# Optimization experiments

Measured on AMD Instinct MI355X. Metric: run time of the kernel, lower is better.

## Reference

```python
import jax, jax.numpy as jnp
import numpy as np

NUM_EMBEDDINGS = 1024
EMBEDDING_DIM = 256
COMMITMENT_COST = 0.25
DECAY = 0.99
EPSILON = 1e-05


def setup_inputs() -> dict:
    key = jax.random.key(0)
    k1, k2, k3 = jax.random.split(key, 3)
    z = jax.random.normal(k1, (32, EMBEDDING_DIM, 32, 32), dtype=jnp.float32)
    codebook = jax.random.normal(k2, (NUM_EMBEDDINGS, EMBEDDING_DIM), dtype=jnp.float32)
    ema_cluster_size = jnp.zeros((NUM_EMBEDDINGS,), dtype=jnp.float32)
    ema_dw = jax.random.normal(k3, (NUM_EMBEDDINGS, EMBEDDING_DIM), dtype=jnp.float32)
    return {"z": z, "codebook": codebook, "ema_cluster_size": ema_cluster_size, "ema_dw": ema_dw}


def reference(z, codebook, ema_cluster_size, ema_dw):
    K, D = codebook.shape
    # (B,C,H,W) -> (B,H,W,C)
    zp = jnp.transpose(z, (0, 2, 3, 1))
    z_flat = zp.reshape(-1, D)  # [N, D]
    N = z_flat.shape[0]

    # squared L2 distances to each code: [N, K]
    distances = (jnp.sum(z_flat ** 2, axis=1, keepdims=True)
                 + jnp.sum(codebook ** 2, axis=1)
                 - 2.0 * z_flat @ codebook.T)
    idx = jnp.argmin(distances, axis=1)  # [N]

    quantized = codebook[idx].reshape(zp.shape)  # [B,H,W,C]

    # training-mode EMA codebook update (one-hot scatter expressed as segment sums)
    counts = jax.ops.segment_sum(jnp.ones((N,), z_flat.dtype), idx, num_segments=K)  # encodings.sum(0)
    dw = jax.ops.segment_sum(z_flat, idx, num_segments=K)                            # encodings.T @ z_flat
    new_cluster_size = ema_cluster_size * DECAY + (1.0 - DECAY) * counts
    new_ema_dw = ema_dw * DECAY + (1.0 - DECAY) * dw
    n = jnp.sum(new_cluster_size)
    cluster_size = (new_cluster_size + EPSILON) / (n + K * EPSILON) * n
    new_codebook = new_ema_dw / cluster_size[:, None]

    commitment_loss = jnp.mean((zp - jax.lax.stop_gradient(quantized)) ** 2)
    loss = COMMITMENT_COST * commitment_loss

    # straight-through estimator
    quantized_st = zp + jax.lax.stop_gradient(quantized - zp)

    avg_probs = counts / N
    perplexity = jnp.exp(-jnp.sum(avg_probs * jnp.log(avg_probs + 1e-10)))

    quantized_out = jnp.transpose(quantized_st, (0, 3, 1, 2))  # back to (B,C,H,W)
    return (quantized_out, loss, perplexity, new_codebook, new_cluster_size, new_ema_dw)
```

## Files before the change

### kernel.cpp

```cpp
#include <hip/hip_runtime.h>
#include <cfloat>
#include <cstdint>

#define B_BATCH 32
#define D_DIM   256
#define HW      1024
#define N_POS   32768
#define K_CODES 1024
#define DECAY_F   0.99f
#define ONE_M_DECAY 0.01f
#define EPS_F   1e-5f

#define OUT_Q    0
#define OUT_LOSS 8388608
#define OUT_PERP 8388609
#define OUT_CB   8388610
#define OUT_NCS  8650754
#define OUT_EDW  8651778


#define WS_COUNTS  0
#define WS_ZNORM   4096
#define WS_BSUM    4100
#define WS_MEMSET  4104
#define WS_CBNORM  4352
#define WS_OFFS    8448
#define WS_CURSOR  12544
#define WS_IDX     16640
#define WS_SORTED  147712
#define WS_CBHI    278784
#define WS_CBLO    803072
#define WS_PART    1327360
#define WS_SCODE   3424512
#define WS_TOTAL   3555584

typedef short s16x8 __attribute__((ext_vector_type(8)));
typedef float f32x4 __attribute__((ext_vector_type(4)));
typedef unsigned long long u64;

__device__ __forceinline__ ushort f2bf_rne(float x) {
    uint u = __float_as_uint(x);
    uint r = (u + 0x7FFF + ((u >> 16) & 1)) >> 16;
    return (ushort)r;
}
__device__ __forceinline__ float bf2f(ushort h) {
    return __uint_as_float(((uint)h) << 16);
}

__device__ __forceinline__ void gload16(const void* g, void* l) {
    __builtin_amdgcn_global_load_lds(
        (const __attribute__((address_space(1))) unsigned*)(uintptr_t)g,
        (__attribute__((address_space(3))) unsigned*)(uintptr_t)l, 16, 0, 0);
}

__global__ __launch_bounds__(256) void prep_ztrans(const float* __restrict__ z,
                                                   const float* __restrict__ cb,
                                                   ushort* __restrict__ zhi,
                                                   ushort* __restrict__ zlo,
                                                   ushort* __restrict__ cbhi,
                                                   ushort* __restrict__ cblo,
                                                   float* __restrict__ cbnorm,
                                                   float* __restrict__ znorm_acc) {
    __shared__ float Zs[32][65];
    __shared__ float red[256];
    const int tid = threadIdx.x;

    if (blockIdx.x >= 512) {
        int wave = tid >> 6;
        int lane = tid & 63;
        int k = (blockIdx.x - 512) * 4 + wave;
        float4 v = *(const float4*)&cb[(size_t)k * D_DIM + lane * 4];
        ushort4 h, l;
        h.x = f2bf_rne(v.x); l.x = f2bf_rne(v.x - bf2f(h.x));
        h.y = f2bf_rne(v.y); l.y = f2bf_rne(v.y - bf2f(h.y));
        h.z = f2bf_rne(v.z); l.z = f2bf_rne(v.z - bf2f(h.z));
        h.w = f2bf_rne(v.w); l.w = f2bf_rne(v.w - bf2f(h.w));
        *(ushort4*)&cbhi[(size_t)k * D_DIM + lane * 4] = h;
        *(ushort4*)&cblo[(size_t)k * D_DIM + lane * 4] = l;
        float s = v.x * v.x + v.y * v.y + v.z * v.z + v.w * v.w;
        #pragma unroll
        for (int off = 32; off >= 1; off >>= 1) s += __shfl_xor(s, off);
        if (lane == 0) cbnorm[k] = s;
        return;
    }

    const int n0  = blockIdx.x * 64;
    const int b   = n0 >> 10;
    const int hw0 = n0 & 1023;
    const float* zb = z + (size_t)b * (D_DIM * HW) + hw0;

    const int zn = tid & 63;
    const int zdb = (tid >> 6) * 8;
    const int n  = tid >> 2;
    const int dq = tid & 3;
    float zsum = 0.f;

    for (int d0 = 0; d0 < D_DIM; d0 += 32) {
        __syncthreads();
        #pragma unroll
        for (int j = 0; j < 8; ++j)
            Zs[zdb + j][zn] = zb[(size_t)(d0 + zdb + j) * HW + zn];
        __syncthreads();
        s16x8 hv, lv;
        #pragma unroll
        for (int j = 0; j < 8; ++j) {
            float f = Zs[dq * 8 + j][n];
            zsum += f * f;
            ushort hb = f2bf_rne(f);
            ushort lb = f2bf_rne(f - bf2f(hb));
            hv[j] = (short)hb;
            lv[j] = (short)lb;
        }
        *(s16x8*)&zhi[(size_t)(n0 + n) * D_DIM + d0 + dq * 8] = hv;
        *(s16x8*)&zlo[(size_t)(n0 + n) * D_DIM + d0 + dq * 8] = lv;
    }
    red[tid] = zsum;
    __syncthreads();
    for (int s2 = 128; s2 >= 1; s2 >>= 1) {
        if (tid < s2) red[tid] += red[tid + s2];
        __syncthreads();
    }
    if (tid == 0) atomicAdd(znorm_acc, red[0]);
}

__global__ __launch_bounds__(256) void argmin_gemm(const ushort* __restrict__ cbhi,
                                                   const ushort* __restrict__ cblo,
                                                   const ushort* __restrict__ zhi,
                                                   const ushort* __restrict__ zlo,
                                                   const float* __restrict__ cbnorm,
                                                   u64* __restrict__ partial) {
    __shared__ ushort lds[16384];
    __shared__ u64 kred[128][2];

    const int tid  = threadIdx.x;
    const int wave = tid >> 6;
    const int lane = tid & 63;
    const int col  = lane & 15;
    const int lg   = lane >> 4;
    const int blk = blockIdx.x;
    const int mt = (blk >> 3) & 7;
    const int pt = (blk & 7) | ((blk >> 6) << 3);
    const int ch = wave & 1;
    const int ph = wave >> 1;

    const int r0  = tid >> 2;
    const int dch = (tid & 3) ^ ((r0 >> 1) & 3);
    const size_t eA0 = (size_t)(mt * 128 + r0) * D_DIM + dch * 8;
    const size_t eB0 = (size_t)(pt * 128 + r0) * D_DIM + dch * 8;
    const int ldsw = wave * 512;

    const int swz = (lg ^ ((col >> 1) & 3)) * 8;
    const int soffA = (ch * 64 + col) * 32 + swz;
    const int soffB = (ph * 64 + col) * 32 + swz;

    f32x4 acc[4][4];
    #pragma unroll
    for (int mi = 0; mi < 4; ++mi)
        #pragma unroll
        for (int ni = 0; ni < 4; ++ni) acc[mi][ni] = {0.f, 0.f, 0.f, 0.f};

    for (int s8 = 0; s8 < 8; ++s8) {
        const int d0 = s8 * 32;
        __syncthreads();
        gload16(cbhi + eA0 + d0,            &lds[0     + ldsw]);
        gload16(cbhi + eA0 + 64 * 256 + d0, &lds[2048  + ldsw]);
        gload16(cblo + eA0 + d0,            &lds[4096  + ldsw]);
        gload16(cblo + eA0 + 64 * 256 + d0, &lds[6144  + ldsw]);
        gload16(zhi  + eB0 + d0,            &lds[8192  + ldsw]);
        gload16(zhi  + eB0 + 64 * 256 + d0, &lds[10240 + ldsw]);
        gload16(zlo  + eB0 + d0,            &lds[12288 + ldsw]);
        gload16(zlo  + eB0 + 64 * 256 + d0, &lds[14336 + ldsw]);
        __syncthreads();

        s16x8 ah[4], al[4], bh[4], bl[4];
        #pragma unroll
        for (int mi = 0; mi < 4; ++mi) {
            int so = soffA + mi * 512;
            ah[mi] = *(const s16x8*)&lds[so];
            al[mi] = *(const s16x8*)&lds[4096 + so];
        }
        #pragma unroll
        for (int ni = 0; ni < 4; ++ni) {
            int so = soffB + ni * 512;
            bh[ni] = *(const s16x8*)&lds[8192 + so];
            bl[ni] = *(const s16x8*)&lds[12288 + so];
        }
        #pragma unroll
        for (int mi = 0; mi < 4; ++mi)
            #pragma unroll
            for (int ni = 0; ni < 4; ++ni) {
                acc[mi][ni] = __builtin_amdgcn_mfma_f32_16x16x32_bf16(ah[mi], bh[ni], acc[mi][ni], 0, 0, 0);
                acc[mi][ni] = __builtin_amdgcn_mfma_f32_16x16x32_bf16(ah[mi], bl[ni], acc[mi][ni], 0, 0, 0);
                acc[mi][ni] = __builtin_amdgcn_mfma_f32_16x16x32_bf16(al[mi], bh[ni], acc[mi][ni], 0, 0, 0);
            }
    }

    const int kbase = mt * 128 + ch * 64;
    u64 best[4] = {~0ull, ~0ull, ~0ull, ~0ull};
    #pragma unroll
    for (int mi = 0; mi < 4; ++mi) {
        float4 cn = *(const float4*)&cbnorm[kbase + mi * 16 + lg * 4];
        const float* cnp = (const float*)&cn;
        #pragma unroll
        for (int ni = 0; ni < 4; ++ni) {
            #pragma unroll
            for (int r = 0; r < 4; ++r) {
                float dist = cnp[r] - 2.f * acc[mi][ni][r];
                uint ub = __float_as_uint(dist);
                ub = ub ^ (uint)(((int)ub >> 31) | 0x80000000);
                u64 key = ((u64)ub << 32) | (uint)(kbase + mi * 16 + lg * 4 + r);
                if (key < best[ni]) best[ni] = key;
            }
        }
    }
    #pragma unroll
    for (int ni = 0; ni < 4; ++ni) {
        u64 o = __shfl_xor(best[ni], 16); if (o < best[ni]) best[ni] = o;
        o = __shfl_xor(best[ni], 32); if (o < best[ni]) best[ni] = o;
    }
    if (lane < 16) {
        #pragma unroll
        for (int ni = 0; ni < 4; ++ni)
            kred[ph * 64 + ni * 16 + lane][ch] = best[ni];
    }
    __syncthreads();
    if (tid < 128) {
        u64 a = kred[tid][0], b = kred[tid][1];
        partial[(size_t)(pt * 128 + tid) * 8 + mt] = a < b ? a : b;
    }
}

__global__ __launch_bounds__(256) void combine_kernel(const u64* __restrict__ partial,
                                                      int* __restrict__ idx,
                                                      float* __restrict__ counts,
                                                      float* __restrict__ bsum_acc) {
    __shared__ int hist[1024];
    __shared__ float red[256];
    const int tid = threadIdx.x;
    for (int j = tid; j < 1024; j += 256) hist[j] = 0;
    __syncthreads();
    int n = blockIdx.x * 256 + tid;
    const u64* p = partial + (size_t)n * 8;
    u64 m = p[0];
    #pragma unroll
    for (int j = 1; j < 8; ++j) { u64 v = p[j]; if (v < m) m = v; }
    int k = (int)(m & 1023u);
    idx[n] = k;
    atomicAdd(&hist[k], 1);
    uint ub = (uint)(m >> 32);
    uint u = (ub & 0x80000000u) ? (ub ^ 0x80000000u) : ~ub;
    red[tid] = __uint_as_float(u);
    __syncthreads();
    for (int s2 = 128; s2 >= 1; s2 >>= 1) {
        if (tid < s2) red[tid] += red[tid + s2];
        __syncthreads();
    }
    if (tid == 0) atomicAdd(bsum_acc, red[0]);
    for (int j = tid; j < 1024; j += 256) {
        int c = hist[j];
        if (c) atomicAdd(&counts[j], (float)c);
    }
}

__global__ __launch_bounds__(1024) void small_kernel(const float* __restrict__ ema_cs,
                                                     const float* __restrict__ counts,
                                                     const float* __restrict__ znorm,
                                                     const float* __restrict__ bsum,
                                                     float* __restrict__ out_ncs,
                                                     float* __restrict__ out_perp,
                                                     float* __restrict__ out_loss,
                                                     float* __restrict__ ntot_ws,
                                                     int* __restrict__ offsets,
                                                     int* __restrict__ cursor) {
    __shared__ float s1[1024];
    __shared__ float s2[1024];
    __shared__ int   s3[1024];
    int k = threadIdx.x;
    float cnt = counts[k];
    float ncs = ema_cs[k] * DECAY_F + ONE_M_DECAY * cnt;
    out_ncs[k] = ncs;
    float p = cnt / (float)N_POS;
    s1[k] = ncs;
    s2[k] = p * logf(p + 1e-10f);
    int c = (int)cnt;
    s3[k] = c;
    __syncthreads();
    for (int off = 1; off < 1024; off <<= 1) {
        int v = (k >= off) ? s3[k - off] : 0;
        __syncthreads();
        s3[k] += v;
        __syncthreads();
    }
    int excl = s3[k] - c;
    offsets[k] = excl;
    cursor[k] = excl;
    for (int st = 512; st >= 1; st >>= 1) {
        if (k < st) { s1[k] += s1[k + st]; s2[k] += s2[k + st]; }
        __syncthreads();
    }
    if (k == 0) {
        ntot_ws[0] = s1[0];
        out_perp[0] = expf(-s2[0]);
        out_loss[0] = 0.25f * (znorm[0] + bsum[0]) / 8388608.0f;
    }
}

__global__ __launch_bounds__(256) void scatter_kernel(const int* __restrict__ idx,
                                                      int* __restrict__ cursor,
                                                      int* __restrict__ sorted,
                                                      int* __restrict__ scode,
                                                      float* __restrict__ dw_zero) {
    __shared__ int hist[1024];
    __shared__ int base_s[1024];
    const int tid = threadIdx.x;
    {
        float4 z4 = {0.f, 0.f, 0.f, 0.f};
        size_t e = ((size_t)blockIdx.x * 256 + tid) * 8;
        *(float4*)&dw_zero[e] = z4;
        *(float4*)&dw_zero[e + 4] = z4;
    }
    for (int j = tid; j < 1024; j += 256) hist[j] = 0;
    __syncthreads();
    int n = blockIdx.x * 256 + tid;
    int k = idx[n];
    atomicAdd(&hist[k], 1);
    __syncthreads();
    for (int j = tid; j < 1024; j += 256) {
        int c = hist[j];
        if (c) base_s[j] = atomicAdd(&cursor[j], c);
        hist[j] = 0;
    }
    __syncthreads();
    int rank = atomicAdd(&hist[k], 1);
    int pos = base_s[k] + rank;
    sorted[pos] = n;
    scode[pos] = k;
}

#define DW_CHUNK 64
__global__ __launch_bounds__(256) void dw_chunk_kernel(const ushort* __restrict__ zhi,
                                                       const ushort* __restrict__ zlo,
                                                       const int* __restrict__ sorted,
                                                       const int* __restrict__ scode,
                                                       const int* __restrict__ offsets,
                                                       const float* __restrict__ counts,
                                                       float* __restrict__ dw) {
    __shared__ int sid[DW_CHUNK];
    __shared__ int sk[DW_CHUNK];
    const int tid = threadIdx.x;
    const int p0 = blockIdx.x * DW_CHUNK;
    if (tid < DW_CHUNK) {
        sid[tid] = sorted[p0 + tid];
        sk[tid]  = scode[p0 + tid];
    }
    __syncthreads();
    float acc = 0.f;
    int runstart = 0;
    #pragma unroll 4
    for (int i = 0; i < DW_CHUNK; ++i) {
        int id = sid[i];
        float zv = bf2f(zhi[(size_t)id * D_DIM + tid]) + bf2f(zlo[(size_t)id * D_DIM + tid]);
        acc += zv;
        bool end = (i == DW_CHUNK - 1) || (sk[i + 1] != sk[i]);
        if (end) {
            int k = sk[i];
            int off = offsets[k];
            int cnt = (int)counts[k];
            if (p0 + runstart == off && p0 + i == off + cnt - 1)
                dw[(size_t)k * D_DIM + tid] = acc;
            else
                atomicAdd(&dw[(size_t)k * D_DIM + tid], acc);
            acc = 0.f;
            runstart = i + 1;
        }
    }
}

__global__ __launch_bounds__(256) void fuse_lite(const float* __restrict__ cb,
                                                 const int* __restrict__ idx,
                                                 float* __restrict__ outq) {
    __shared__ float Qs[32][65];
    __shared__ int kidx[64];
    const int tid = threadIdx.x;
    const int n0  = blockIdx.x * 64;
    const int b   = n0 >> 10;
    const int hw0 = n0 & 1023;
    float* ob = outq + (size_t)b * (D_DIM * HW) + hw0;

    if (tid < 64) kidx[tid] = idx[n0 + tid];

    for (int d0 = 0; d0 < D_DIM; d0 += 32) {
        __syncthreads();
        #pragma unroll
        for (int h = 0; h < 2; ++h) {
            int s  = tid + 256 * h;
            int n  = s >> 3;
            int dq = s & 7;
            int k  = kidx[n];
            float4 q = *(const float4*)&cb[(size_t)k * D_DIM + d0 + dq * 4];
            Qs[dq * 4 + 0][n] = q.x;
            Qs[dq * 4 + 1][n] = q.y;
            Qs[dq * 4 + 2][n] = q.z;
            Qs[dq * 4 + 3][n] = q.w;
        }
        __syncthreads();
        #pragma unroll
        for (int j = 0; j < 8; ++j) {
            int v = tid + 256 * j;
            int d = v >> 6;
            int n = v & 63;
            ob[(size_t)(d0 + d) * HW + n] = Qs[d][n];
        }
    }
}

__global__ __launch_bounds__(256) void finalize_rows(const float* __restrict__ ema_dw,
                                                     const float* __restrict__ out_ncs,
                                                     const float* __restrict__ ntot_ws,
                                                     float* __restrict__ out_edw,
                                                     float* __restrict__ out_cb) {
    int k = blockIdx.x;
    int d = threadIdx.x;
    float ncs = out_ncs[k];
    float nt = ntot_ws[0];
    float csz = (ncs + EPS_F) / (nt + (float)K_CODES * EPS_F) * nt;
    size_t e = (size_t)k * D_DIM + d;
    float ed = ema_dw[e] * DECAY_F + ONE_M_DECAY * out_edw[e];
    out_edw[e] = ed;
    out_cb[e] = ed / csz;
}

extern "C" void kernel_launch(void* const* d_in, const int* in_sizes, int n_in,
                              void* d_out, int out_size, void* d_ws, size_t ws_size,
                              hipStream_t stream) {
    const float* z       = (const float*)d_in[0];
    const float* cb      = (const float*)d_in[1];
    const float* ema_cs  = (const float*)d_in[2];
    const float* ema_dw  = (const float*)d_in[3];
    float* out = (float*)d_out;

    char* ws = (char*)d_ws;
    float* ws_counts = (float*)(ws + WS_COUNTS);
    float* ws_znorm  = (float*)(ws + WS_ZNORM);
    float* ws_bsum   = (float*)(ws + WS_BSUM);
    float* ws_cbnorm = (float*)(ws + WS_CBNORM);
    int*   ws_offs   = (int*)(ws + WS_OFFS);
    int*   ws_cursor = (int*)(ws + WS_CURSOR);
    int*   ws_idx    = (int*)(ws + WS_IDX);
    int*   ws_sorted = (int*)(ws + WS_SORTED);
    ushort* ws_cbhi  = (ushort*)(ws + WS_CBHI);
    ushort* ws_cblo  = (ushort*)(ws + WS_CBLO);
    u64*   ws_part   = (u64*)(ws + WS_PART);
    int*   ws_scode  = (int*)(ws + WS_SCODE);

    ushort* zhi = (ushort*)out;
    ushort* zlo = zhi + 8388608;

    hipMemsetAsync(d_ws, 0, WS_MEMSET, stream);

    prep_ztrans<<<768, 256, 0, stream>>>(z, cb, zhi, zlo, ws_cbhi, ws_cblo,
                                         ws_cbnorm, ws_znorm);
    argmin_gemm<<<2048, 256, 0, stream>>>(ws_cbhi, ws_cblo, zhi, zlo, ws_cbnorm, ws_part);
    combine_kernel<<<N_POS / 256, 256, 0, stream>>>(ws_part, ws_idx, ws_counts, ws_bsum);
    small_kernel<<<1, 1024, 0, stream>>>(ema_cs, ws_counts, ws_znorm, ws_bsum,
                                         out + OUT_NCS, out + OUT_PERP, out + OUT_LOSS,
                                         (float*)(ws + WS_ZNORM) + 1024, ws_offs, ws_cursor);
    scatter_kernel<<<N_POS / 256, 256, 0, stream>>>(ws_idx, ws_cursor, ws_sorted,
                                                    ws_scode, out + OUT_EDW);
    dw_chunk_kernel<<<N_POS / DW_CHUNK, 256, 0, stream>>>(zhi, zlo, ws_sorted, ws_scode,
                                                          ws_offs, ws_counts, out + OUT_EDW);
    fuse_lite<<<N_POS / 64, 256, 0, stream>>>(cb, ws_idx, out + OUT_Q);
    finalize_rows<<<K_CODES, 256, 0, stream>>>(ema_dw, out + OUT_NCS,
                                               (float*)(ws + WS_ZNORM) + 1024,
                                               out + OUT_EDW, out + OUT_CB);
}
```

Baseline: 216.1 us.

## Triple-buffer argmin GEMM with larger 256x128 tiles and 512-thread blocks

Restructures the split-bf16 distance GEMM to use 512-thread blocks covering 256 codes by 128 positions, with K-steps of 32 bf16 elements. Global-to-LDS loads go through a three-stage ring buffer using explicit vmcnt waits and raw barriers, so loads for later steps overlap with MFMA work. MFMA sections also run at raised wave priority. Each position now has half as many partial argmin candidates, so the combine kernel reads 4 instead of 8. The cost is about 144KB of LDS per block, which limits occupancy, and more fragile hand-written wait counts.

```diff
diff --git a/kernel.cpp b/kernel.cpp
--- a/kernel.cpp
+++ b/kernel.cpp
@@ -123,35 +123,49 @@
     if (tid == 0) atomicAdd(znorm_acc, red[0]);
 }
 
-__global__ __launch_bounds__(256) void argmin_gemm(const ushort* __restrict__ cbhi,
-                                                   const ushort* __restrict__ cblo,
-                                                   const ushort* __restrict__ zhi,
-                                                   const ushort* __restrict__ zlo,
-                                                   const float* __restrict__ cbnorm,
-                                                   u64* __restrict__ partial) {
-    __shared__ ushort lds[16384];
-    __shared__ u64 kred[128][2];
+__global__ __launch_bounds__(512, 2) void argmin_gemm(const ushort* __restrict__ cbhi,
+                                                      const ushort* __restrict__ cblo,
+                                                      const ushort* __restrict__ zhi,
+                                                      const ushort* __restrict__ zlo,
+                                                      const float* __restrict__ cbnorm,
+                                                      u64* __restrict__ partial) {
+    __shared__ __align__(16) ushort lds[73728];
 
     const int tid  = threadIdx.x;
     const int wave = tid >> 6;
     const int lane = tid & 63;
     const int col  = lane & 15;
     const int lg   = lane >> 4;
-    const int blk = blockIdx.x;
-    const int mt = (blk >> 3) & 7;
-    const int pt = (blk & 7) | ((blk >> 6) << 3);
-    const int ch = wave & 1;
-    const int ph = wave >> 1;
-
-    const int r0  = tid >> 2;
-    const int dch = (tid & 3) ^ ((r0 >> 1) & 3);
-    const size_t eA0 = (size_t)(mt * 128 + r0) * D_DIM + dch * 8;
-    const size_t eB0 = (size_t)(pt * 128 + r0) * D_DIM + dch * 8;
-    const int ldsw = wave * 512;
-
-    const int swz = (lg ^ ((col >> 1) & 3)) * 8;
-    const int soffA = (ch * 64 + col) * 32 + swz;
-    const int soffB = (ph * 64 + col) * 32 + swz;
+    const int wr   = wave >> 1;
+    const int wc   = wave & 1;
+    const int blk  = blockIdx.x;
+    const int mt = (blk >> 3) & 3;
+    const int pt = (blk & 7) | ((blk >> 5) << 3);
+
+    const int srow = tid >> 2;
+    const int G    = tid & 3;
+    const int sg   = (G ^ ((srow >> 1) & 3)) * 16;
+    const char* pAh = (const char*)cbhi + (size_t)(mt * 256 + srow) * 512 + sg;
+    const char* pAl = (const char*)cblo + (size_t)(mt * 256 + srow) * 512 + sg;
+    const char* pBh = (const char*)zhi  + (size_t)(pt * 128 + srow) * 512 + sg;
+    const char* pBl = (const char*)zlo  + (size_t)(pt * 128 + srow) * 512 + sg;
+    char* const ldsw = (char*)lds + wave * 1024;
+
+    auto stage = [&](int kt, int bsel) {
+        char* d = ldsw + bsel * 49152;
+        const int kb = kt * 64;
+        gload16(pAh + kb,         d);
+        gload16(pAh + kb + 65536, d + 8192);
+        gload16(pAl + kb,         d + 16384);
+        gload16(pAl + kb + 65536, d + 24576);
+        gload16(pBh + kb,         d + 32768);
+        gload16(pBl + kb,         d + 40960);
+    };
+
+    const char* ldsc = (const char*)lds;
+    const int swz  = (lg ^ ((col >> 1) & 3)) * 16;
+    const int aoff = (wr * 64 + col) * 64 + swz;
+    const int boff = (wc * 64 + col) * 64 + swz;
 
     f32x4 acc[4][4];
     #pragma unroll
@@ -159,32 +173,31 @@
         #pragma unroll
         for (int ni = 0; ni < 4; ++ni) acc[mi][ni] = {0.f, 0.f, 0.f, 0.f};
 
-    for (int s8 = 0; s8 < 8; ++s8) {
-        const int d0 = s8 * 32;
-        __syncthreads();
-        gload16(cbhi + eA0 + d0,            &lds[0     + ldsw]);
-        gload16(cbhi + eA0 + 64 * 256 + d0, &lds[2048  + ldsw]);
-        gload16(cblo + eA0 + d0,            &lds[4096  + ldsw]);
-        gload16(cblo + eA0 + 64 * 256 + d0, &lds[6144  + ldsw]);
-        gload16(zhi  + eB0 + d0,            &lds[8192  + ldsw]);
-        gload16(zhi  + eB0 + 64 * 256 + d0, &lds[10240 + ldsw]);
-        gload16(zlo  + eB0 + d0,            &lds[12288 + ldsw]);
-        gload16(zlo  + eB0 + 64 * 256 + d0, &lds[14336 + ldsw]);
-        __syncthreads();
-
+    stage(0, 0);
+    stage(1, 1);
+
+    #pragma unroll
+    for (int t = 0; t < 8; ++t) {
+        const int cur = t % 3;
+        if (t < 7) asm volatile("s_waitcnt vmcnt(6)" ::: "memory");
+        else       asm volatile("s_waitcnt vmcnt(0)" ::: "memory");
+        __builtin_amdgcn_s_barrier();
+        __builtin_amdgcn_sched_barrier(0);
+        if (t < 6) stage(t + 2, (t + 2) % 3);
+
+        const int base = cur * 49152;
         s16x8 ah[4], al[4], bh[4], bl[4];
         #pragma unroll
         for (int mi = 0; mi < 4; ++mi) {
-            int so = soffA + mi * 512;
-            ah[mi] = *(const s16x8*)&lds[so];
-            al[mi] = *(const s16x8*)&lds[4096 + so];
+            ah[mi] = *(const s16x8*)(ldsc + base + aoff + mi * 1024);
+            al[mi] = *(const s16x8*)(ldsc + base + 16384 + aoff + mi * 1024);
         }
         #pragma unroll
         for (int ni = 0; ni < 4; ++ni) {
-            int so = soffB + ni * 512;
-            bh[ni] = *(const s16x8*)&lds[8192 + so];
-            bl[ni] = *(const s16x8*)&lds[12288 + so];
-        }
+            bh[ni] = *(const s16x8*)(ldsc + base + 32768 + boff + ni * 1024);
+            bl[ni] = *(const s16x8*)(ldsc + base + 40960 + boff + ni * 1024);
+        }
+        __builtin_amdgcn_s_setprio(1);
         #pragma unroll
         for (int mi = 0; mi < 4; ++mi)
             #pragma unroll
@@ -193,9 +206,10 @@
                 acc[mi][ni] = __builtin_amdgcn_mfma_f32_16x16x32_bf16(ah[mi], bl[ni], acc[mi][ni], 0, 0, 0);
                 acc[mi][ni] = __builtin_amdgcn_mfma_f32_16x16x32_bf16(al[mi], bh[ni], acc[mi][ni], 0, 0, 0);
             }
-    }
-
-    const int kbase = mt * 128 + ch * 64;
+        __builtin_amdgcn_s_setprio(0);
+    }
+
+    const int kbase = mt * 256 + wr * 64;
     u64 best[4] = {~0ull, ~0ull, ~0ull, ~0ull};
     #pragma unroll
     for (int mi = 0; mi < 4; ++mi) {
@@ -218,15 +232,19 @@
         u64 o = __shfl_xor(best[ni], 16); if (o < best[ni]) best[ni] = o;
         o = __shfl_xor(best[ni], 32); if (o < best[ni]) best[ni] = o;
     }
+    u64* kredp = (u64*)lds;
     if (lane < 16) {
         #pragma unroll
         for (int ni = 0; ni < 4; ++ni)
-            kred[ph * 64 + ni * 16 + lane][ch] = best[ni];
+            kredp[(wc * 64 + ni * 16 + lane) * 4 + wr] = best[ni];
     }
     __syncthreads();
     if (tid < 128) {
-        u64 a = kred[tid][0], b = kred[tid][1];
-        partial[(size_t)(pt * 128 + tid) * 8 + mt] = a < b ? a : b;
+        u64 a = kredp[tid * 4 + 0];
+        u64 b = kredp[tid * 4 + 1]; if (b < a) a = b;
+        b = kredp[tid * 4 + 2]; if (b < a) a = b;
+        b = kredp[tid * 4 + 3]; if (b < a) a = b;
+        partial[(size_t)(pt * 128 + tid) * 4 + mt] = a;
     }
 }
 
@@ -240,10 +258,10 @@
     for (int j = tid; j < 1024; j += 256) hist[j] = 0;
     __syncthreads();
     int n = blockIdx.x * 256 + tid;
-    const u64* p = partial + (size_t)n * 8;
+    const u64* p = partial + (size_t)n * 4;
     u64 m = p[0];
     #pragma unroll
-    for (int j = 1; j < 8; ++j) { u64 v = p[j]; if (v < m) m = v; }
+    for (int j = 1; j < 4; ++j) { u64 v = p[j]; if (v < m) m = v; }
     int k = (int)(m & 1023u);
     idx[n] = k;
     atomicAdd(&hist[k], 1);
@@ -460,7 +478,7 @@
 
     prep_ztrans<<<768, 256, 0, stream>>>(z, cb, zhi, zlo, ws_cbhi, ws_cblo,
                                          ws_cbnorm, ws_znorm);
-    argmin_gemm<<<2048, 256, 0, stream>>>(ws_cbhi, ws_cblo, zhi, zlo, ws_cbnorm, ws_part);
+    argmin_gemm<<<1024, 512, 0, stream>>>(ws_cbhi, ws_cblo, zhi, zlo, ws_cbnorm, ws_part);
     combine_kernel<<<N_POS / 256, 256, 0, stream>>>(ws_part, ws_idx, ws_counts, ws_bsum);
     small_kernel<<<1, 1024, 0, stream>>>(ema_cs, ws_counts, ws_znorm, ws_bsum,
                                          out + OUT_NCS, out + OUT_PERP, out + OUT_LOSS,
```

Measured after the change: 209.6 us. -3.0%, faster.
